# Kernel optimization log

Hardware: AMD Instinct MI355X
Metric: run time of the kernel (lower is better)

## Reference

```python
import jax, jax.numpy as jnp
import numpy as np

B, C_IN, C_OUT, H, W = 8, 256, 256, 48, 48


def setup_inputs() -> dict:
    key = jax.random.key(0)
    ks = jax.random.split(key, 8)
    s = 1.0 / np.sqrt(C_IN)
    return {
        "x1": jax.random.normal(ks[0], (B, C_IN, H, W), dtype=jnp.float32),
        "x2": jax.random.normal(ks[1], (B, C_IN, H, W), dtype=jnp.float32),
        "Wq": jax.random.normal(ks[2], (C_OUT, C_IN), dtype=jnp.float32) * s,
        "bq": jax.random.normal(ks[3], (C_OUT,), dtype=jnp.float32) * s,
        "Wk": jax.random.normal(ks[4], (C_OUT, C_IN), dtype=jnp.float32) * s,
        "bk": jax.random.normal(ks[5], (C_OUT,), dtype=jnp.float32) * s,
        "Wv": jax.random.normal(ks[6], (C_OUT, C_IN), dtype=jnp.float32) * s,
        "bv": jax.random.normal(ks[7], (C_OUT,), dtype=jnp.float32) * s,
    }


def _conv1x1(x, Wt, b):
    # x: [B,Cin,H,W], Wt: [Cout,Cin] -> [B,Cout,H,W]
    return jnp.einsum("bchw,oc->bohw", x, Wt) + b[None, :, None, None]


def reference(x1, x2, Wq, bq, Wk, bk, Wv, bv):
    q = _conv1x1(x1, Wq, bq)  # [B,C,H,W]
    k = _conv1x1(x2, Wk, bk)
    v = _conv1x1(x2, Wv, bv)
    b, c, h, w = q.shape
    n = h * w
    qf = q.reshape(b, c, n).transpose(0, 2, 1)  # [B,N,C]
    kf = k.reshape(b, c, n)                      # [B,C,N]
    vf = v.reshape(b, c, n).transpose(0, 2, 1)   # [B,N,C]
    # NOTE: faithful to source -- no 1/sqrt(d) scaling, no head split
    attn = jax.nn.softmax(jnp.einsum("bic,bcj->bij", qf, kf), axis=-1)  # [B,N,N]
    out = jnp.einsum("bij,bjc->bic", attn, vf)   # [B,N,C]
    return out.transpose(0, 2, 1).reshape(b, c, h, w)
```

## Files before the change

### kernel.cpp

```cpp
#include <hip/hip_runtime.h>
#include <cfloat>
#include <cstddef>
#include <cstdint>

#define BATCH 8
#define CDIM  256
#define NTOK  2304

typedef float    f32x4 __attribute__((ext_vector_type(4)));
typedef _Float16 f16x8 __attribute__((ext_vector_type(8)));
typedef _Float16 f16x4 __attribute__((ext_vector_type(4)));

#define MFMA16(a, b, c) __builtin_amdgcn_mfma_f32_16x16x32_f16(a, b, c, 0, 0, 0)

__device__ __forceinline__ void gl_lds16(const void* g, void* l) {
    __builtin_amdgcn_global_load_lds(
        (const __attribute__((address_space(1))) void*)g,
        (__attribute__((address_space(3))) void*)l, 16, 0, 0);
}

__global__ __launch_bounds__(256) void cast_fused(
    const float* __restrict__ x1, const float* __restrict__ x2,
    const float* __restrict__ Wq, const float* __restrict__ Wk,
    const float* __restrict__ Wv,
    _Float16* __restrict__ Xt1, _Float16* __restrict__ Xt2,
    _Float16* __restrict__ Wh)
{
    const int tid = threadIdx.x;
    int bx = blockIdx.x;

    if (bx < 192) {
        int i = (bx * 256 + tid) * 4;
        const float* src = (i < 65536) ? (Wq + i)
                         : (i < 131072) ? (Wk + (i - 65536)) : (Wv + (i - 131072));
        float4 v = *(const float4*)src;
        f16x4 h = { (_Float16)v.x, (_Float16)v.y, (_Float16)v.z, (_Float16)v.w };
        *(f16x4*)(Wh + i) = h;
        return;
    }
    bx -= 192;
    const int n0 = (bx % 36) * 64;
    const int rest = bx / 36;
    const int c0 = (rest & 3) * 64;
    const int bz = rest >> 2;
    const float* X   = (bz < 8) ? x1 : x2;
    _Float16*   Xt   = (bz < 8) ? Xt1 : Xt2;
    const int b = bz & 7;

    __shared__ _Float16 T[64][72];

    {
        const int cl = tid >> 2, nch = (tid & 3) * 16;
        const float* src = X + (size_t)(b * CDIM + c0 + cl) * NTOK + n0 + nch;
#pragma unroll
        for (int u = 0; u < 4; ++u) {
            float4 v = *(const float4*)(src + u * 4);
            T[cl][nch + u * 4 + 0] = (_Float16)v.x;
            T[cl][nch + u * 4 + 1] = (_Float16)v.y;
            T[cl][nch + u * 4 + 2] = (_Float16)v.z;
            T[cl][nch + u * 4 + 3] = (_Float16)v.w;
        }
    }
    __syncthreads();
    {
        const int nl = tid >> 2, cch = (tid & 3) * 16;
        _Float16* dst = Xt + (size_t)(b * NTOK + n0 + nl) * CDIM + c0 + cch;
        f16x8 o0, o1;
#pragma unroll
        for (int i = 0; i < 8; ++i) {
            o0[i] = T[cch + i][nl];
            o1[i] = T[cch + 8 + i][nl];
        }
        *(f16x8*)dst = o0;
        *(f16x8*)(dst + 8) = o1;
    }
}

__global__ __launch_bounds__(256, 2) void proj_mfma(
    const _Float16* __restrict__ Xt1, const _Float16* __restrict__ Xt2,
    const _Float16* __restrict__ Wh,
    const float* __restrict__ bq, const float* __restrict__ bk,
    const float* __restrict__ bv,
    _Float16* __restrict__ Qo, _Float16* __restrict__ Ko, _Float16* __restrict__ Vo)
{
    const int tid  = threadIdx.x;
    const int lane = tid & 63;
    const int w    = tid >> 6;
    const int l15  = lane & 15, l4 = lane >> 4;
    const int n0   = blockIdx.x * 64;
    const int mode = blockIdx.y;
    const int b    = blockIdx.z;

    const _Float16* Xt = (mode == 0) ? Xt1 : Xt2;
    const _Float16* Wm = Wh + mode * 65536;
    const float* bias  = (mode == 0) ? bq : (mode == 1) ? bk : bv;
    _Float16* OUT      = (mode == 0) ? Qo : (mode == 1) ? Ko : Vo;

    __shared__ __align__(16) char sm[65536];
    _Float16* Xl = (_Float16*)sm;
    _Float16* Wl = (_Float16*)(sm + 32768);

#pragma unroll
    for (int t = 0; t < 8; ++t) {
        int i = w * 8 + t;
        int row = 2 * i + (lane >> 5);
        int ch  = lane & 31;
        gl_lds16(Xt + (size_t)(b * NTOK + n0 + row) * CDIM + ((ch ^ (row & 7)) * 8),
                 (char*)Xl + i * 1024);
    }

    float bias_o[4];
#pragma unroll
    for (int ot = 0; ot < 4; ++ot) bias_o[ot] = bias[w * 64 + ot * 16 + l15];

    f32x4 acc[16];
#pragma unroll
    for (int i = 0; i < 16; ++i) acc[i] = (f32x4){0.f, 0.f, 0.f, 0.f};

    for (int c0 = 0; c0 < CDIM; c0 += 64) {
        __syncthreads();
#pragma unroll
        for (int t = 0; t < 8; ++t) {
            int i = w * 8 + t;
            int row = 8 * i + (lane >> 3);
            int ch  = lane & 7;
            gl_lds16(Wm + (size_t)row * CDIM + c0 + ((ch ^ (row & 7)) * 8),
                     (char*)Wl + i * 1024);
        }
        __syncthreads();

#pragma unroll
        for (int kk2 = 0; kk2 < 2; ++kk2) {
            f16x8 a[4], bf[4];
#pragma unroll
            for (int nt = 0; nt < 4; ++nt) {
                int row = nt * 16 + l15;
                int ch  = ((c0 >> 3) + kk2 * 4 + l4) ^ (row & 7);
                a[nt] = *(const f16x8*)((const char*)Xl + row * 512 + ch * 16);
            }
#pragma unroll
            for (int ot = 0; ot < 4; ++ot) {
                int row = w * 64 + ot * 16 + l15;
                int ch  = (kk2 * 4 + l4) ^ (row & 7);
                bf[ot] = *(const f16x8*)((const char*)Wl + row * 128 + ch * 16);
            }
#pragma unroll
            for (int nt = 0; nt < 4; ++nt)
#pragma unroll
                for (int ot = 0; ot < 4; ++ot)
                    acc[nt * 4 + ot] = MFMA16(a[nt], bf[ot], acc[nt * 4 + ot]);
        }
    }

    __syncthreads();

    if (mode <= 1) {
        _Float16* Dl = (_Float16*)sm;
#pragma unroll
        for (int nt = 0; nt < 4; ++nt)
#pragma unroll
            for (int ot = 0; ot < 4; ++ot)
#pragma unroll
                for (int reg = 0; reg < 4; ++reg)
                    Dl[(nt * 16 + 4 * l4 + reg) * 256 + w * 64 + ot * 16 + l15] =
                        (_Float16)(acc[nt * 4 + ot][reg] + bias_o[ot]);
        __syncthreads();
        char* dst = (char*)(OUT + ((size_t)b * NTOK + n0) * CDIM);
#pragma unroll
        for (int u = 0; u < 8; ++u) {
            f16x8 v = *(const f16x8*)((const char*)Dl + u * 4096 + tid * 16);
            *(f16x8*)(dst + u * 4096 + tid * 16) = v;
        }
    } else {
        _Float16* Dlv = (_Float16*)sm;
#pragma unroll
        for (int nt = 0; nt < 4; ++nt)
#pragma unroll
            for (int ot = 0; ot < 4; ++ot)
#pragma unroll
                for (int reg = 0; reg < 4; ++reg)
                    Dlv[(w * 64 + ot * 16 + l15) * 80 + nt * 16 + 4 * l4 + reg] =
                        (_Float16)(acc[nt * 4 + ot][reg] + bias_o[ot]);
        __syncthreads();
#pragma unroll
        for (int t = 0; t < 8; ++t) {
            int ro = (w * 8 + t) * 8 + (lane >> 3);
            f16x8 v = *(const f16x8*)((const char*)Dlv + ro * 160 + (lane & 7) * 16);
            *(f16x8*)(OUT + ((size_t)b * CDIM + ro) * NTOK + n0 + (lane & 7) * 8) = v;
        }
    }
}

template <int SEG>
__global__ __launch_bounds__(512, 2) void attn_fa(
    const _Float16* __restrict__ Q, const _Float16* __restrict__ K,
    const _Float16* __restrict__ Vt, _Float16* __restrict__ pacc,
    float2* __restrict__ pml)
{
    const int tid  = threadIdx.x;
    const int lane = tid & 63;
    const int w    = tid >> 6;
    const int l15  = lane & 15, l4 = lane >> 4;

    const int nb  = 18 * BATCH * SEG, cpx = nb / 8;
    const int bid = blockIdx.x;
    const int swz = (bid & 7) * cpx + (bid >> 3);
    const int x = swz % 18;
    const int b = (swz / 18) & 7;
    const int z = swz / 144;

    const int row0   = x * 128 + w * 16;
    const int jbase  = z * (NTOK / SEG);
    const int NTILES = NTOK / SEG / 64;

    __shared__ __align__(16) char smem[131072];

    const size_t kbb = (size_t)b * NTOK;
    const size_t vbb = (size_t)b * CDIM * NTOK;

    auto stage = [&](int j0, int buf) {
        char* Klc = smem + buf * 65536;
        char* Vlc = Klc + 32768;
#pragma unroll
        for (int t = 0; t < 4; ++t) {
            int i  = w * 4 + t;
            int lr = 2 * i + (lane >> 5);
            int gr = (lr & 32) | ((lr & 12) << 1) | ((lr & 16) >> 2) | (lr & 3);
            int chunk = lane & 31;
            gl_lds16(K + (kbb + j0 + gr) * CDIM + ((chunk ^ (lr & 7)) * 8),
                     Klc + i * 1024);
        }
#pragma unroll
        for (int t = 0; t < 4; ++t) {
            int i = w * 4 + t;
            int vrow = 8 * i + (lane >> 3);
            int chunk = lane & 7;
            gl_lds16(Vt + vbb + (size_t)vrow * NTOK + j0 + ((chunk ^ (vrow & 7)) * 8),
                     Vlc + i * 1024);
        }
    };

    f16x8 qa[8];
    {
        const _Float16* qb = Q + ((size_t)b * NTOK + row0 + l15) * CDIM + l4 * 8;
#pragma unroll
        for (int kk = 0; kk < 8; ++kk)
            qa[kk] = __builtin_nontemporal_load((const f16x8*)(qb + kk * 32));
    }

    f32x4 acc[16];
#pragma unroll
    for (int ct = 0; ct < 16; ++ct) acc[ct] = (f32x4){0.f, 0.f, 0.f, 0.f};
    f32x4 accl = (f32x4){0.f, 0.f, 0.f, 0.f};
    float m = -FLT_MAX;

    const f16x8 vone = {(_Float16)1.f, (_Float16)1.f, (_Float16)1.f, (_Float16)1.f,
                        (_Float16)1.f, (_Float16)1.f, (_Float16)1.f, (_Float16)1.f};

    stage(jbase, 0);
    __syncthreads();

    for (int jt = 0; jt < NTILES; ++jt) {
        const int cur = jt & 1;

        if (jt + 1 < NTILES) stage(jbase + (jt + 1) * 64, cur ^ 1);

        const char* Klc = (const char*)smem + cur * 65536;
        const char* Vlc = Klc + 32768;

        f32x4 s[4];
        __builtin_amdgcn_s_setprio(1);
#pragma unroll
        for (int nt = 0; nt < 4; ++nt) {
            const char* kb = Klc + (nt * 16 + l15) * 512;
            f32x4 sv = (f32x4){0.f, 0.f, 0.f, 0.f};
#pragma unroll
            for (int kk = 0; kk < 8; ++kk) {
                f16x8 kf = *(const f16x8*)(kb + (((kk * 4 + l4) ^ (l15 & 7)) * 16));
                sv = MFMA16(kf, qa[kk], sv);
            }
            s[nt] = sv;
        }
        __builtin_amdgcn_s_setprio(0);

        float pm = fmaxf(fmaxf(s[0][0], s[0][1]), fmaxf(s[0][2], s[0][3]));
        pm = fmaxf(pm, fmaxf(fmaxf(s[1][0], s[1][1]), fmaxf(s[1][2], s[1][3])));
        pm = fmaxf(pm, fmaxf(fmaxf(s[2][0], s[2][1]), fmaxf(s[2][2], s[2][3])));
        pm = fmaxf(pm, fmaxf(fmaxf(s[3][0], s[3][1]), fmaxf(s[3][2], s[3][3])));
        pm = fmaxf(pm, __shfl_xor(pm, 16));
        pm = fmaxf(pm, __shfl_xor(pm, 32));
        if (pm > m + 8.f) {
            float sc = __expf(m - pm);
            m = pm;
#pragma unroll
            for (int e = 0; e < 4; ++e) accl[e] *= sc;
#pragma unroll
            for (int ct = 0; ct < 16; ++ct)
#pragma unroll
                for (int e = 0; e < 4; ++e) acc[ct][e] *= sc;
        }

        f16x8 pa[2];
#pragma unroll
        for (int kc = 0; kc < 2; ++kc)
#pragma unroll
            for (int e = 0; e < 8; ++e)
                pa[kc][e] = (_Float16)__expf(s[2 * kc + (e >> 2)][e & 3] - m);

        __builtin_amdgcn_s_setprio(1);
        accl = MFMA16(vone, pa[0], accl);
        accl = MFMA16(vone, pa[1], accl);
#pragma unroll
        for (int ct = 0; ct < 16; ++ct) {
            const char* vb0 = Vlc + (ct * 16 + l15) * 128;
#pragma unroll
            for (int kc = 0; kc < 2; ++kc) {
                f16x8 vb = *(const f16x8*)(vb0 + (((kc * 4 + l4) ^ (l15 & 7)) * 16));
                acc[ct] = MFMA16(vb, pa[kc], acc[ct]);
            }
        }
        __builtin_amdgcn_s_setprio(0);

        __syncthreads();
    }

    _Float16* stg = (_Float16*)(smem + w * 8448);
    {
        float inv = 1.f / accl[0];
#pragma unroll
        for (int ct = 0; ct < 16; ++ct) {
            f16x4 o = { (_Float16)(acc[ct][0] * inv), (_Float16)(acc[ct][1] * inv),
                        (_Float16)(acc[ct][2] * inv), (_Float16)(acc[ct][3] * inv) };
            *(f16x4*)&stg[l15 * 264 + ct * 16 + l4 * 4] = o;
        }
        if (l4 == 0)
            pml[((size_t)z * BATCH + b) * NTOK + row0 + l15] =
                make_float2(m, accl[0]);
    }
    asm volatile("s_waitcnt lgkmcnt(0)" ::: "memory");
    __builtin_amdgcn_sched_barrier(0);
    {
        const char* stgc = (const char*)stg;
        char* dst = (char*)(pacc + ((size_t)z * BATCH + b) * NTOK * CDIM
                            + (size_t)row0 * CDIM);
#pragma unroll
        for (int u = 0; u < 8; ++u) {
            int r = 2 * u + (lane >> 5);
            f16x8 v = *(const f16x8*)(stgc + r * 528 + (lane & 31) * 16);
            *(f16x8*)(dst + r * 512 + (lane & 31) * 16) = v;
        }
    }
}

template <int SEG>
__global__ __launch_bounds__(256) void merge_kernel(
    const _Float16* __restrict__ pacc, const float2* __restrict__ pml,
    float* __restrict__ out)
{
    const int tid = threadIdx.x;
    const int n0 = blockIdx.x * 64;
    const int cc = blockIdx.y;
    const int b  = blockIdx.z;

    __shared__ float wgt[SEG][64];
    __shared__ float dinv[64];
    __shared__ float T[64][68];

    if (tid < 64) {
        int n = n0 + tid;
        float ms[SEG], ls[SEG];
#pragma unroll
        for (int s = 0; s < SEG; ++s) {
            float2 v = pml[((size_t)s * BATCH + b) * NTOK + n];
            ms[s] = v.x; ls[s] = v.y;
        }
        float M = ms[0];
#pragma unroll
        for (int s = 1; s < SEG; ++s) M = fmaxf(M, ms[s]);
        float den = 0.f;
#pragma unroll
        for (int s = 0; s < SEG; ++s) {
            float g = ls[s] * __expf(ms[s] - M);
            wgt[s][tid] = g;
            den += g;
        }
        dinv[tid] = 1.f / den;
    }
    __syncthreads();

    {
        const int nl = tid >> 2, cg = (tid & 3) * 16;
        float a[16];
#pragma unroll
        for (int u = 0; u < 16; ++u) a[u] = 0.f;
#pragma unroll
        for (int s = 0; s < SEG; ++s) {
            const _Float16* p = pacc + (((size_t)s * BATCH + b) * NTOK + n0 + nl) * CDIM
                                + cc * 64 + cg;
            f16x8 v0 = ((const f16x8*)p)[0];
            f16x8 v1 = ((const f16x8*)p)[1];
            float g = wgt[s][nl];
#pragma unroll
            for (int u = 0; u < 8; ++u) {
                a[u]     += g * (float)v0[u];
                a[8 + u] += g * (float)v1[u];
            }
        }
        float di = dinv[nl];
#pragma unroll
        for (int u = 0; u < 16; ++u) T[nl][cg + u] = a[u] * di;
    }
    __syncthreads();
    {
        const int cl = tid >> 2, nb2 = (tid & 3) * 16;
        float* ob = out + ((size_t)b * CDIM + cc * 64 + cl) * NTOK + n0 + nb2;
#pragma unroll
        for (int u = 0; u < 4; ++u) {
            float4 v = { T[nb2 + u * 4 + 0][cl], T[nb2 + u * 4 + 1][cl],
                         T[nb2 + u * 4 + 2][cl], T[nb2 + u * 4 + 3][cl] };
            *(float4*)&ob[u * 4] = v;
        }
    }
}

extern "C" void kernel_launch(void* const* d_in, const int* in_sizes, int n_in,
                              void* d_out, int out_size, void* d_ws, size_t ws_size,
                              hipStream_t stream)
{
    const float* x1 = (const float*)d_in[0];
    const float* x2 = (const float*)d_in[1];
    const float* Wq = (const float*)d_in[2];
    const float* bq = (const float*)d_in[3];
    const float* Wk = (const float*)d_in[4];
    const float* bk = (const float*)d_in[5];
    const float* Wv = (const float*)d_in[6];
    const float* bv = (const float*)d_in[7];
    float* out = (float*)d_out;

    const size_t plane = (size_t)BATCH * NTOK * CDIM;
    _Float16* ws16 = (_Float16*)d_ws;
    _Float16* Q   = ws16;
    _Float16* K   = ws16 + plane;
    _Float16* Vt  = ws16 + 2 * plane;
    _Float16* Xt1 = ws16 + 3 * plane;
    _Float16* Xt2 = ws16 + 4 * plane;
    _Float16* Wh  = ws16 + 5 * plane;
    const size_t fixed16 = 5 * plane + 196608;

    auto need = [&](size_t S) {
        return fixed16 * 2 + S * plane * 2 + S * (size_t)BATCH * NTOK * 8;
    };
    const int SEG = (ws_size >= need(3)) ? 3 : (ws_size >= need(2)) ? 2 : 1;

    _Float16* pacc = ws16 + fixed16;
    float2*   pml  = (float2*)((char*)d_ws + fixed16 * 2 + (size_t)SEG * plane * 2);

    cast_fused<<<dim3(192 + 36 * 4 * 16), dim3(256), 0, stream>>>(
        x1, x2, Wq, Wk, Wv, Xt1, Xt2, Wh);
    proj_mfma<<<dim3(36, 3, BATCH), dim3(256), 0, stream>>>(
        Xt1, Xt2, Wh, bq, bk, bv, Q, K, Vt);

    const int nb = 18 * BATCH;
    if (SEG == 3) {
        attn_fa<3><<<dim3(nb * 3), dim3(512), 0, stream>>>(Q, K, Vt, pacc, pml);
        merge_kernel<3><<<dim3(36, 4, BATCH), dim3(256), 0, stream>>>(pacc, pml, out);
    } else if (SEG == 2) {
        attn_fa<2><<<dim3(nb * 2), dim3(512), 0, stream>>>(Q, K, Vt, pacc, pml);
        merge_kernel<2><<<dim3(36, 4, BATCH), dim3(256), 0, stream>>>(pacc, pml, out);
    } else {
        attn_fa<1><<<dim3(nb), dim3(512), 0, stream>>>(Q, K, Vt, pacc, pml);
        merge_kernel<1><<<dim3(36, 4, BATCH), dim3(256), 0, stream>>>(pacc, pml, out);
    }
}
```

Measured before the change: 116.1 us.

## Switch attention kernel to 32x32x16 MFMA with 256-row query tiles

```diff
diff --git a/kernel.cpp b/kernel.cpp
--- a/kernel.cpp
+++ b/kernel.cpp
@@ -7,11 +7,13 @@
 #define CDIM  256
 #define NTOK  2304
 
-typedef float    f32x4 __attribute__((ext_vector_type(4)));
-typedef _Float16 f16x8 __attribute__((ext_vector_type(8)));
-typedef _Float16 f16x4 __attribute__((ext_vector_type(4)));
+typedef float    f32x4  __attribute__((ext_vector_type(4)));
+typedef float    f32x16 __attribute__((ext_vector_type(16)));
+typedef _Float16 f16x8  __attribute__((ext_vector_type(8)));
+typedef _Float16 f16x4  __attribute__((ext_vector_type(4)));
 
 #define MFMA16(a, b, c) __builtin_amdgcn_mfma_f32_16x16x32_f16(a, b, c, 0, 0, 0)
+#define MFMA32(a, b, c) __builtin_amdgcn_mfma_f32_32x32x16_f16(a, b, c, 0, 0, 0)
 
 __device__ __forceinline__ void gl_lds16(const void* g, void* l) {
     __builtin_amdgcn_global_load_lds(
@@ -200,16 +202,17 @@
     const int tid  = threadIdx.x;
     const int lane = tid & 63;
     const int w    = tid >> 6;
-    const int l15  = lane & 15, l4 = lane >> 4;
-
-    const int nb  = 18 * BATCH * SEG, cpx = nb / 8;
+    const int l31  = lane & 31;
+    const int h    = lane >> 5;
+
+    const int nb  = 9 * BATCH * SEG, cpx = nb / 8;
     const int bid = blockIdx.x;
     const int swz = (bid & 7) * cpx + (bid >> 3);
-    const int x = swz % 18;
-    const int b = (swz / 18) & 7;
-    const int z = swz / 144;
-
-    const int row0   = x * 128 + w * 16;
+    const int x = swz % 9;
+    const int b = (swz / 9) & 7;
+    const int z = swz / 72;
+
+    const int row0   = x * 256 + w * 32;
     const int jbase  = z * (NTOK / SEG);
     const int NTILES = NTOK / SEG / 64;
 
@@ -225,7 +228,7 @@
         for (int t = 0; t < 4; ++t) {
             int i  = w * 4 + t;
             int lr = 2 * i + (lane >> 5);
-            int gr = (lr & 32) | ((lr & 12) << 1) | ((lr & 16) >> 2) | (lr & 3);
+            int gr = (lr & 51) | ((lr & 4) << 1) | ((lr & 8) >> 1);
             int chunk = lane & 31;
             gl_lds16(K + (kbb + j0 + gr) * CDIM + ((chunk ^ (lr & 7)) * 8),
                      Klc + i * 1024);
@@ -240,22 +243,21 @@
         }
     };
 
-    f16x8 qa[8];
+    f16x8 qa[16];
     {
-        const _Float16* qb = Q + ((size_t)b * NTOK + row0 + l15) * CDIM + l4 * 8;
-#pragma unroll
-        for (int kk = 0; kk < 8; ++kk)
-            qa[kk] = __builtin_nontemporal_load((const f16x8*)(qb + kk * 32));
-    }
-
-    f32x4 acc[16];
-#pragma unroll
-    for (int ct = 0; ct < 16; ++ct) acc[ct] = (f32x4){0.f, 0.f, 0.f, 0.f};
-    f32x4 accl = (f32x4){0.f, 0.f, 0.f, 0.f};
-    float m = -FLT_MAX;
-
-    const f16x8 vone = {(_Float16)1.f, (_Float16)1.f, (_Float16)1.f, (_Float16)1.f,
-                        (_Float16)1.f, (_Float16)1.f, (_Float16)1.f, (_Float16)1.f};
+        const _Float16* qb = Q + ((size_t)b * NTOK + row0 + l31) * CDIM + h * 8;
+#pragma unroll
+        for (int kk = 0; kk < 16; ++kk)
+            qa[kk] = __builtin_nontemporal_load((const f16x8*)(qb + kk * 16));
+    }
+
+    f32x16 acc[8];
+#pragma unroll
+    for (int cb = 0; cb < 8; ++cb)
+#pragma unroll
+        for (int e = 0; e < 16; ++e) acc[cb][e] = 0.f;
+    float m  = -FLT_MAX;
+    float ps = 0.f;
 
     stage(jbase, 0);
     __syncthreads();
@@ -268,88 +270,90 @@
         const char* Klc = (const char*)smem + cur * 65536;
         const char* Vlc = Klc + 32768;
 
-        f32x4 s[4];
-        __builtin_amdgcn_s_setprio(1);
-#pragma unroll
-        for (int nt = 0; nt < 4; ++nt) {
-            const char* kb = Klc + (nt * 16 + l15) * 512;
-            f32x4 sv = (f32x4){0.f, 0.f, 0.f, 0.f};
-#pragma unroll
-            for (int kk = 0; kk < 8; ++kk) {
-                f16x8 kf = *(const f16x8*)(kb + (((kk * 4 + l4) ^ (l15 & 7)) * 16));
-                sv = MFMA16(kf, qa[kk], sv);
-            }
-            s[nt] = sv;
-        }
-        __builtin_amdgcn_s_setprio(0);
-
-        float pm = fmaxf(fmaxf(s[0][0], s[0][1]), fmaxf(s[0][2], s[0][3]));
-        pm = fmaxf(pm, fmaxf(fmaxf(s[1][0], s[1][1]), fmaxf(s[1][2], s[1][3])));
-        pm = fmaxf(pm, fmaxf(fmaxf(s[2][0], s[2][1]), fmaxf(s[2][2], s[2][3])));
-        pm = fmaxf(pm, fmaxf(fmaxf(s[3][0], s[3][1]), fmaxf(s[3][2], s[3][3])));
-        pm = fmaxf(pm, __shfl_xor(pm, 16));
-        pm = fmaxf(pm, __shfl_xor(pm, 32));
-        if (pm > m + 8.f) {
-            float sc = __expf(m - pm);
-            m = pm;
-#pragma unroll
-            for (int e = 0; e < 4; ++e) accl[e] *= sc;
-#pragma unroll
-            for (int ct = 0; ct < 16; ++ct)
-#pragma unroll
-                for (int e = 0; e < 4; ++e) acc[ct][e] *= sc;
-        }
-
-        f16x8 pa[2];
-#pragma unroll
-        for (int kc = 0; kc < 2; ++kc)
-#pragma unroll
-            for (int e = 0; e < 8; ++e)
-                pa[kc][e] = (_Float16)__expf(s[2 * kc + (e >> 2)][e & 3] - m);
-
-        __builtin_amdgcn_s_setprio(1);
-        accl = MFMA16(vone, pa[0], accl);
-        accl = MFMA16(vone, pa[1], accl);
-#pragma unroll
-        for (int ct = 0; ct < 16; ++ct) {
-            const char* vb0 = Vlc + (ct * 16 + l15) * 128;
-#pragma unroll
-            for (int kc = 0; kc < 2; ++kc) {
-                f16x8 vb = *(const f16x8*)(vb0 + (((kc * 4 + l4) ^ (l15 & 7)) * 16));
-                acc[ct] = MFMA16(vb, pa[kc], acc[ct]);
-            }
-        }
-        __builtin_amdgcn_s_setprio(0);
+#pragma unroll
+        for (int jb = 0; jb < 2; ++jb) {
+            f32x16 s;
+#pragma unroll
+            for (int e = 0; e < 16; ++e) s[e] = 0.f;
+            const char* kb = Klc + (jb * 32 + l31) * 512;
+#pragma unroll
+            for (int kk = 0; kk < 16; ++kk) {
+                f16x8 kf = *(const f16x8*)(kb + (((kk * 2 + h) ^ (l31 & 7)) * 16));
+                s = MFMA32(kf, qa[kk], s);
+            }
+
+            float pm = s[0];
+#pragma unroll
+            for (int e = 1; e < 16; ++e) pm = fmaxf(pm, s[e]);
+            pm = fmaxf(pm, __shfl_xor(pm, 32));
+            if (pm > m + 8.f) {
+                float sc = __expf(m - pm);
+                m = pm;
+                ps *= sc;
+#pragma unroll
+                for (int cb = 0; cb < 8; ++cb)
+#pragma unroll
+                    for (int e = 0; e < 16; ++e) acc[cb][e] *= sc;
+            }
+
+            f16x8 pa0, pa1;
+#pragma unroll
+            for (int e = 0; e < 8; ++e) {
+                float p0 = __expf(s[e] - m);
+                float p1 = __expf(s[8 + e] - m);
+                ps += p0 + p1;
+                pa0[e] = (_Float16)p0;
+                pa1[e] = (_Float16)p1;
+            }
+
+#pragma unroll
+            for (int cb = 0; cb < 8; ++cb) {
+                const char* vb0 = Vlc + (cb * 32 + l31) * 128;
+                f16x8 v0 = *(const f16x8*)(vb0 + (((jb * 4 + 0 + h) ^ (l31 & 7)) * 16));
+                acc[cb] = MFMA32(v0, pa0, acc[cb]);
+                f16x8 v1 = *(const f16x8*)(vb0 + (((jb * 4 + 2 + h) ^ (l31 & 7)) * 16));
+                acc[cb] = MFMA32(v1, pa1, acc[cb]);
+            }
+        }
 
         __syncthreads();
     }
 
+    float l_full = ps + __shfl_xor(ps, 32);
+    float inv = 1.f / l_full;
+    const size_t pbase = ((size_t)z * BATCH + b) * NTOK * CDIM;
     _Float16* stg = (_Float16*)(smem + w * 8448);
-    {
-        float inv = 1.f / accl[0];
-#pragma unroll
-        for (int ct = 0; ct < 16; ++ct) {
-            f16x4 o = { (_Float16)(acc[ct][0] * inv), (_Float16)(acc[ct][1] * inv),
-                        (_Float16)(acc[ct][2] * inv), (_Float16)(acc[ct][3] * inv) };
-            *(f16x4*)&stg[l15 * 264 + ct * 16 + l4 * 4] = o;
-        }
-        if (l4 == 0)
-            pml[((size_t)z * BATCH + b) * NTOK + row0 + l15] =
-                make_float2(m, accl[0]);
-    }
-    asm volatile("s_waitcnt lgkmcnt(0)" ::: "memory");
-    __builtin_amdgcn_sched_barrier(0);
-    {
-        const char* stgc = (const char*)stg;
-        char* dst = (char*)(pacc + ((size_t)z * BATCH + b) * NTOK * CDIM
-                            + (size_t)row0 * CDIM);
-#pragma unroll
-        for (int u = 0; u < 8; ++u) {
-            int r = 2 * u + (lane >> 5);
-            f16x8 v = *(const f16x8*)(stgc + r * 528 + (lane & 31) * 16);
-            *(f16x8*)(dst + r * 512 + (lane & 31) * 16) = v;
-        }
-    }
+
+#pragma unroll
+    for (int pass = 0; pass < 2; ++pass) {
+#pragma unroll
+        for (int cb4 = 0; cb4 < 4; ++cb4) {
+            const f32x16 a = acc[pass * 4 + cb4];
+#pragma unroll
+            for (int g = 0; g < 4; ++g) {
+                f16x4 o = { (_Float16)(a[4 * g + 0] * inv),
+                            (_Float16)(a[4 * g + 1] * inv),
+                            (_Float16)(a[4 * g + 2] * inv),
+                            (_Float16)(a[4 * g + 3] * inv) };
+                *(f16x4*)&stg[l31 * 132 + cb4 * 32 + g * 8 + h * 4] = o;
+            }
+        }
+        asm volatile("s_waitcnt lgkmcnt(0)" ::: "memory");
+        __builtin_amdgcn_sched_barrier(0);
+        {
+            char* dst = (char*)(pacc + pbase + (size_t)row0 * CDIM) + pass * 256;
+#pragma unroll
+            for (int u = 0; u < 8; ++u) {
+                int r = u * 4 + (lane >> 4);
+                f16x8 v = *(const f16x8*)((const char*)stg + r * 264 + (lane & 15) * 16);
+                *(f16x8*)(dst + (size_t)r * 512 + (lane & 15) * 16) = v;
+            }
+        }
+        asm volatile("s_waitcnt lgkmcnt(0)" ::: "memory");
+        __builtin_amdgcn_sched_barrier(0);
+    }
+    if (lane < 32)
+        pml[((size_t)z * BATCH + b) * NTOK + row0 + lane] = make_float2(m, l_full);
 }
 
 template <int SEG>
@@ -460,7 +464,7 @@
     proj_mfma<<<dim3(36, 3, BATCH), dim3(256), 0, stream>>>(
         Xt1, Xt2, Wh, bq, bk, bv, Q, K, Vt);
 
-    const int nb = 18 * BATCH;
+    const int nb = 9 * BATCH;
     if (SEG == 3) {
         attn_fa<3><<<dim3(nb * 3), dim3(512), 0, stream>>>(Q, K, Vt, pacc, pml);
         merge_kernel<3><<<dim3(36, 4, BATCH), dim3(256), 0, stream>>>(pacc, pml, out);
```

New measurement: 142.7 us. 1.23x slower.
